# Kernel tuning notes

Measured on AMD Instinct MI355X. Metric: run time of the kernel, lower is better.

Reference implementation:

```python
import jax, jax.numpy as jnp
import numpy as np

N_POINTS = 8388608  # 8M points


def setup_inputs() -> dict:
    key = jax.random.key(0)
    k1, k2 = jax.random.split(key)
    pcloud = jax.random.normal(k1, (1, N_POINTS, 3), dtype=jnp.float32)
    P1 = jax.random.normal(k2, (3,), dtype=jnp.float32)
    return {"pcloud": pcloud, "P1": P1, "K": 64}


def reference(pcloud, P1, K):
    # pcloud: (1, N, 3) -> (N, 3); P1: (3,) -> (1, 3)
    pts = pcloud.reshape(-1, 3)
    diff = pts - P1.reshape(1, 3)
    dist = jnp.sqrt(jnp.sum(diff * diff, axis=1))  # L2 distance per point, (N,)
    # torch.topk(largest=False) == top_k on negated distances
    _, idx = jax.lax.top_k(-dist, K)  # (K,)
    return pts[idx], idx.reshape(1, -1)
```

## Files before the change

kernel.cpp:

```cpp
#include <hip/hip_runtime.h>
#include <stdint.h>

#define NBINS 4096
#define NB2   4096
#define NBLK  2048
#define SLOT  16
#define OVF_CAP 8192
#define LDS_CAND 8192
#define SAMP_PTS 131072
#define SBLK 128
#define CHUNK_PTS 256
#define CHUNK_F4  192

__device__ __forceinline__ uint32_t dist_key(float x, float y, float z,
                                             float px, float py, float pz) {
    float dx = __fsub_rn(x, px);
    float dy = __fsub_rn(y, py);
    float dz = __fsub_rn(z, pz);
    float s = __fadd_rn(__fadd_rn(__fmul_rn(dx, dx), __fmul_rn(dy, dy)),
                        __fmul_rn(dz, dz));
    float d = __fsqrt_rn(s);
    return __float_as_uint(d);
}

__global__ void __launch_bounds__(256) sample_scan_kernel(
        const float* __restrict__ pts, const float* __restrict__ P1,
        uint32_t* __restrict__ ghist, uint32_t* __restrict__ cutp,
        uint32_t* __restrict__ done_s, int nsamp, int K) {
    __shared__ uint32_t lh[NBINS];
    __shared__ uint32_t ssum[256];
    __shared__ int is_last;
    for (int i = threadIdx.x; i < NBINS; i += 256) lh[i] = 0;
    __syncthreads();
    float px = P1[0], py = P1[1], pz = P1[2];
    int gid = blockIdx.x * 256 + threadIdx.x;
    const float4* p4 = (const float4*)pts;
    if (gid * 4 < nsamp) {
        float4 A = p4[gid * 3 + 0];
        float4 Bv = p4[gid * 3 + 1];
        float4 Cv = p4[gid * 3 + 2];
        atomicAdd(&lh[dist_key(A.x, A.y, A.z, px, py, pz) >> 20], 1u);
        atomicAdd(&lh[dist_key(A.w, Bv.x, Bv.y, px, py, pz) >> 20], 1u);
        atomicAdd(&lh[dist_key(Bv.z, Bv.w, Cv.x, px, py, pz) >> 20], 1u);
        atomicAdd(&lh[dist_key(Cv.y, Cv.z, Cv.w, px, py, pz) >> 20], 1u);
    }
    __syncthreads();
    for (int i = threadIdx.x; i < NBINS; i += 256) {
        uint32_t v = lh[i];
        if (v) atomicAdd(&ghist[i], v);
    }
    __syncthreads();
    if (threadIdx.x == 0) {
        asm volatile("s_waitcnt vmcnt(0)" ::: "memory");
        uint32_t old = __hip_atomic_fetch_add(done_s, 1u, __ATOMIC_RELAXED,
                                              __HIP_MEMORY_SCOPE_AGENT);
        is_last = (old == (uint32_t)(gridDim.x - 1));
    }
    __syncthreads();
    if (!is_last) return;

    int t = threadIdx.x;
    uint32_t mine[16];
    uint32_t local = 0;
    for (int j = 0; j < 16; ++j) {
        mine[j] = __hip_atomic_load(&ghist[t * 16 + j], __ATOMIC_RELAXED,
                                    __HIP_MEMORY_SCOPE_AGENT);
        local += mine[j];
    }
    ssum[t] = local;
    __syncthreads();
    for (int off = 1; off < 256; off <<= 1) {
        uint32_t v = (t >= off) ? ssum[t - off] : 0;
        __syncthreads();
        ssum[t] += v;
        __syncthreads();
    }
    uint32_t incl = ssum[t];
    uint32_t excl = incl - local;
    if (excl < (uint32_t)K && incl >= (uint32_t)K) {
        uint32_t run = excl;
        for (int j = 0; j < 16; ++j) {
            run += mine[j];
            if (run >= (uint32_t)K) { *cutp = (uint32_t)(t * 16 + j); break; }
        }
    }
}

__global__ void __launch_bounds__(256) filter_kernel(
        const float* __restrict__ pts, const float* __restrict__ P1,
        const uint32_t* __restrict__ cutp,
        unsigned long long* __restrict__ gslots,
        uint32_t* __restrict__ gcount,
        uint32_t* __restrict__ ovf_cnt, unsigned long long* __restrict__ ovf,
        int nchunks, int N) {
    __shared__ float4 park[4][CHUNK_F4];
    __shared__ unsigned long long lhits[SLOT];
    __shared__ uint32_t lcnt;
    if (threadIdx.x == 0) lcnt = 0;
    __syncthreads();

    const float4* p4 = (const float4*)pts;
    float px = P1[0], py = P1[1], pz = P1[2];
    uint32_t cb = *cutp;
    int w = threadIdx.x >> 6;
    int lane = threadIdx.x & 63;
    int b = blockIdx.x;
    int cpb = (nchunks + NBLK - 1) / NBLK;
    int cbeg = b * cpb;
    int cend = cbeg + cpb; if (cend > nchunks) cend = nchunks;

    float4 a0, a1, a2, b0, b1, b2;
    int c = cbeg + w;
    bool hasA = (c < cend);
    if (hasA) {
        const float4* s = p4 + (size_t)c * CHUNK_F4;
        a0 = s[lane]; a1 = s[lane + 64]; a2 = s[lane + 128];
    }
    bool hasB = (c + 4 < cend);
    if (hasB) {
        const float4* s = p4 + (size_t)(c + 4) * CHUNK_F4;
        b0 = s[lane]; b1 = s[lane + 64]; b2 = s[lane + 128];
    }
    while (hasA) {
        park[w][lane] = a0; park[w][lane + 64] = a1; park[w][lane + 128] = a2;
        bool loadA = (c + 8 < cend);
        if (loadA) {
            const float4* s = p4 + (size_t)(c + 8) * CHUNK_F4;
            a0 = s[lane]; a1 = s[lane + 64]; a2 = s[lane + 128];
        }
        asm volatile("s_waitcnt lgkmcnt(0)" ::: "memory");
        {
            const float* fb = (const float*)&park[w][0] + lane * 12;
            float4 A  = *(const float4*)(fb);
            float4 Bv = *(const float4*)(fb + 4);
            float4 Cv = *(const float4*)(fb + 8);
            uint32_t kk[4];
            kk[0] = dist_key(A.x, A.y, A.z, px, py, pz);
            kk[1] = dist_key(A.w, Bv.x, Bv.y, px, py, pz);
            kk[2] = dist_key(Bv.z, Bv.w, Cv.x, px, py, pz);
            kk[3] = dist_key(Cv.y, Cv.z, Cv.w, px, py, pz);
            uint32_t pbase = (uint32_t)c * CHUNK_PTS + (uint32_t)lane * 4;
            #pragma unroll
            for (int j = 0; j < 4; ++j) {
                if ((kk[j] >> 20) <= cb) {
                    unsigned long long cv = ((unsigned long long)kk[j] << 32) |
                                            (unsigned long long)(pbase + j);
                    uint32_t pos = atomicAdd(&lcnt, 1u);
                    if (pos < SLOT) lhits[pos] = cv;
                    else {
                        uint32_t op = atomicAdd(ovf_cnt, 1u);
                        if (op < OVF_CAP) ovf[op] = cv;
                    }
                }
            }
        }
        bool loadB = false;
        if (hasB) {
            park[w][lane] = b0; park[w][lane + 64] = b1; park[w][lane + 128] = b2;
            loadB = (c + 12 < cend);
            if (loadB) {
                const float4* s = p4 + (size_t)(c + 12) * CHUNK_F4;
                b0 = s[lane]; b1 = s[lane + 64]; b2 = s[lane + 128];
            }
            asm volatile("s_waitcnt lgkmcnt(0)" ::: "memory");
            const float* fb = (const float*)&park[w][0] + lane * 12;
            float4 A  = *(const float4*)(fb);
            float4 Bv = *(const float4*)(fb + 4);
            float4 Cv = *(const float4*)(fb + 8);
            uint32_t kk[4];
            kk[0] = dist_key(A.x, A.y, A.z, px, py, pz);
            kk[1] = dist_key(A.w, Bv.x, Bv.y, px, py, pz);
            kk[2] = dist_key(Bv.z, Bv.w, Cv.x, px, py, pz);
            kk[3] = dist_key(Cv.y, Cv.z, Cv.w, px, py, pz);
            uint32_t pbase = (uint32_t)(c + 4) * CHUNK_PTS + (uint32_t)lane * 4;
            #pragma unroll
            for (int j = 0; j < 4; ++j) {
                if ((kk[j] >> 20) <= cb) {
                    unsigned long long cv = ((unsigned long long)kk[j] << 32) |
                                            (unsigned long long)(pbase + j);
                    uint32_t pos = atomicAdd(&lcnt, 1u);
                    if (pos < SLOT) lhits[pos] = cv;
                    else {
                        uint32_t op = atomicAdd(ovf_cnt, 1u);
                        if (op < OVF_CAP) ovf[op] = cv;
                    }
                }
            }
        }
        c += 8;
        hasA = (c < cend);
        hasB = loadB;
    }
    if (b == NBLK - 1 && threadIdx.x == 0) {
        for (int i = nchunks * CHUNK_PTS; i < N; ++i) {
            uint32_t kk = dist_key(pts[3 * i], pts[3 * i + 1], pts[3 * i + 2], px, py, pz);
            if ((kk >> 20) <= cb) {
                unsigned long long cv = ((unsigned long long)kk << 32) |
                                        (unsigned long long)(uint32_t)i;
                uint32_t pos = atomicAdd(&lcnt, 1u);
                if (pos < SLOT) lhits[pos] = cv;
                else {
                    uint32_t op = atomicAdd(ovf_cnt, 1u);
                    if (op < OVF_CAP) ovf[op] = cv;
                }
            }
        }
    }
    __syncthreads();
    uint32_t n = lcnt; if (n > SLOT) n = SLOT;
    if (threadIdx.x < n) gslots[(size_t)b * SLOT + threadIdx.x] = lhits[threadIdx.x];
    if (threadIdx.x == 0) gcount[b] = n;
}

__global__ void __launch_bounds__(1024) refine_select_kernel(
        const uint32_t* __restrict__ gcount,
        const unsigned long long* __restrict__ gslots,
        const uint32_t* __restrict__ ovf_cnt,
        const unsigned long long* __restrict__ ovf,
        const uint32_t* __restrict__ cutp,
        unsigned long long* __restrict__ cand2,
        const float* __restrict__ pts,
        float* __restrict__ out, int K) {
    __shared__ uint32_t hist2[NB2];
    __shared__ uint32_t ssum[1024];
    __shared__ unsigned long long lcand[LDS_CAND];
    __shared__ uint32_t cut2_s, m2_s;
    int t = threadIdx.x;
    uint32_t cb = *cutp;
    unsigned long long R = ((unsigned long long)(cb + 1)) << 20;
    uint32_t M32 = (uint32_t)((((unsigned long long)NB2) << 32) / R);
    uint32_t novf = *ovf_cnt; if (novf > OVF_CAP) novf = OVF_CAP;

    for (int i = t; i < NB2; i += 1024) hist2[i] = 0;
    if (t == 0) { m2_s = 0; cut2_s = NB2 - 1; }
    __syncthreads();
    for (int b = t; b < NBLK; b += 1024) {
        uint32_t n = gcount[b]; if (n > SLOT) n = SLOT;
        for (uint32_t j = 0; j < n; ++j) {
            uint32_t key = (uint32_t)(gslots[(size_t)b * SLOT + j] >> 32);
            atomicAdd(&hist2[(uint32_t)(((unsigned long long)key * M32) >> 32)], 1u);
        }
    }
    for (uint32_t i = t; i < novf; i += 1024) {
        uint32_t key = (uint32_t)(ovf[i] >> 32);
        atomicAdd(&hist2[(uint32_t)(((unsigned long long)key * M32) >> 32)], 1u);
    }
    __syncthreads();

    uint32_t mine[4];
    uint32_t local = 0;
    for (int j = 0; j < 4; ++j) { mine[j] = hist2[t * 4 + j]; local += mine[j]; }
    ssum[t] = local;
    __syncthreads();
    for (int off = 1; off < 1024; off <<= 1) {
        uint32_t v = (t >= off) ? ssum[t - off] : 0;
        __syncthreads();
        ssum[t] += v;
        __syncthreads();
    }
    uint32_t incl = ssum[t], excl = incl - local;
    if (excl < (uint32_t)K && incl >= (uint32_t)K) {
        uint32_t run = excl;
        for (int j = 0; j < 4; ++j) {
            run += mine[j];
            if (run >= (uint32_t)K) { cut2_s = (uint32_t)(t * 4 + j); break; }
        }
    }
    __syncthreads();
    uint32_t c2 = cut2_s;

    for (int b = t; b < NBLK; b += 1024) {
        uint32_t n = gcount[b]; if (n > SLOT) n = SLOT;
        for (uint32_t j = 0; j < n; ++j) {
            unsigned long long cv = gslots[(size_t)b * SLOT + j];
            uint32_t key = (uint32_t)(cv >> 32);
            if ((uint32_t)(((unsigned long long)key * M32) >> 32) <= c2) {
                uint32_t pos = atomicAdd(&m2_s, 1u);
                if (pos < LDS_CAND) lcand[pos] = cv;
                cand2[pos] = cv;
            }
        }
    }
    for (uint32_t i = t; i < novf; i += 1024) {
        unsigned long long cv = ovf[i];
        uint32_t key = (uint32_t)(cv >> 32);
        if ((uint32_t)(((unsigned long long)key * M32) >> 32) <= c2) {
            uint32_t pos = atomicAdd(&m2_s, 1u);
            if (pos < LDS_CAND) lcand[pos] = cv;
            cand2[pos] = cv;
        }
    }
    __syncthreads();
    uint32_t M2 = m2_s;

    if (M2 <= LDS_CAND) {
        for (uint32_t i = t; i < M2; i += 1024) {
            unsigned long long ci = lcand[i];
            uint32_t rank = 0;
            for (uint32_t j = 0; j < M2; ++j) rank += (lcand[j] < ci) ? 1u : 0u;
            if (rank < (uint32_t)K) {
                uint32_t idx = (uint32_t)(ci & 0xFFFFFFFFu);
                out[3 * rank + 0] = pts[3 * idx + 0];
                out[3 * rank + 1] = pts[3 * idx + 1];
                out[3 * rank + 2] = pts[3 * idx + 2];
                out[3 * K + rank] = (float)idx;
            }
        }
    } else {
        for (uint32_t i = t; i < M2; i += 1024) {
            unsigned long long ci = cand2[i];
            uint32_t rank = 0;
            for (uint32_t j = 0; j < M2; ++j) rank += (cand2[j] < ci) ? 1u : 0u;
            if (rank < (uint32_t)K) {
                uint32_t idx = (uint32_t)(ci & 0xFFFFFFFFu);
                out[3 * rank + 0] = pts[3 * idx + 0];
                out[3 * rank + 1] = pts[3 * idx + 1];
                out[3 * rank + 2] = pts[3 * idx + 2];
                out[3 * K + rank] = (float)idx;
            }
        }
    }
}

extern "C" void kernel_launch(void* const* d_in, const int* in_sizes, int n_in,
                              void* d_out, int out_size, void* d_ws, size_t ws_size,
                              hipStream_t stream) {
    const float* pts = (const float*)d_in[0];
    const float* P1  = (const float*)d_in[1];
    float* out = (float*)d_out;

    int N = in_sizes[0] / 3;
    int nchunks = N / CHUNK_PTS;
    int K = out_size / 4;
    int nsamp = (N < SAMP_PTS) ? (N / 4) * 4 : SAMP_PTS;

    uint32_t* w       = (uint32_t*)d_ws;
    uint32_t* ovf_cnt = w + 0;
    uint32_t* cutp    = w + 1;
    uint32_t* done_s  = w + 2;
    uint32_t* hist    = w + 4;
    uint32_t* gcount  = w + 4 + NBINS;
    unsigned long long* gslots = (unsigned long long*)(w + 4 + NBINS + NBLK);
    unsigned long long* ovf    = gslots + (size_t)NBLK * SLOT;
    unsigned long long* cand2  = ovf + OVF_CAP;

    hipMemsetAsync(w, 0, (size_t)(4 + NBINS) * sizeof(uint32_t), stream);
    sample_scan_kernel<<<SBLK, 256, 0, stream>>>(pts, P1, hist, cutp, done_s, nsamp, K);
    filter_kernel<<<NBLK, 256, 0, stream>>>(pts, P1, cutp, gslots, gcount,
                                            ovf_cnt, ovf, nchunks, N);
    refine_select_kernel<<<1, 1024, 0, stream>>>(gcount, gslots, ovf_cnt, ovf,
                                                 cutp, cand2, pts, out, K);
}
```

Baseline: 47.94 us.

## Stream filter chunks via direct global-to-LDS loads with triple-buffered ring

Replaces the register-staged double-buffered loads in the filter kernel with direct global-to-LDS loads into a per-wave three-slot ring, synchronised with vmcnt waits. This drops the register round trip and the explicit LDS stores, and keeps two chunks in flight while the current one is processed. It raises LDS use per block and relies on exact vmcnt accounting and on the wave-uniform LDS addressing semantics of the load-to-LDS instruction.

```diff
diff --git a/kernel.cpp b/kernel.cpp
--- a/kernel.cpp
+++ b/kernel.cpp
@@ -11,6 +11,9 @@
 #define SBLK 128
 #define CHUNK_PTS 256
 #define CHUNK_F4  192
+
+typedef const __attribute__((address_space(1))) void* gas_ptr;
+typedef __attribute__((address_space(3))) void* las_ptr;
 
 __device__ __forceinline__ uint32_t dist_key(float x, float y, float z,
                                              float px, float py, float pz) {
@@ -93,7 +96,7 @@
         uint32_t* __restrict__ gcount,
         uint32_t* __restrict__ ovf_cnt, unsigned long long* __restrict__ ovf,
         int nchunks, int N) {
-    __shared__ float4 park[4][CHUNK_F4];
+    __shared__ float4 ring[4][3][CHUNK_F4];
     __shared__ unsigned long long lhits[SLOT];
     __shared__ uint32_t lcnt;
     if (threadIdx.x == 0) lcnt = 0;
@@ -109,87 +112,50 @@
     int cbeg = b * cpb;
     int cend = cbeg + cpb; if (cend > nchunks) cend = nchunks;
 
-    float4 a0, a1, a2, b0, b1, b2;
-    int c = cbeg + w;
-    bool hasA = (c < cend);
-    if (hasA) {
-        const float4* s = p4 + (size_t)c * CHUNK_F4;
-        a0 = s[lane]; a1 = s[lane + 64]; a2 = s[lane + 128];
-    }
-    bool hasB = (c + 4 < cend);
-    if (hasB) {
-        const float4* s = p4 + (size_t)(c + 4) * CHUNK_F4;
-        b0 = s[lane]; b1 = s[lane + 64]; b2 = s[lane + 128];
-    }
-    while (hasA) {
-        park[w][lane] = a0; park[w][lane + 64] = a1; park[w][lane + 128] = a2;
-        bool loadA = (c + 8 < cend);
-        if (loadA) {
-            const float4* s = p4 + (size_t)(c + 8) * CHUNK_F4;
-            a0 = s[lane]; a1 = s[lane + 64]; a2 = s[lane + 128];
-        }
-        asm volatile("s_waitcnt lgkmcnt(0)" ::: "memory");
-        {
-            const float* fb = (const float*)&park[w][0] + lane * 12;
-            float4 A  = *(const float4*)(fb);
-            float4 Bv = *(const float4*)(fb + 4);
-            float4 Cv = *(const float4*)(fb + 8);
-            uint32_t kk[4];
-            kk[0] = dist_key(A.x, A.y, A.z, px, py, pz);
-            kk[1] = dist_key(A.w, Bv.x, Bv.y, px, py, pz);
-            kk[2] = dist_key(Bv.z, Bv.w, Cv.x, px, py, pz);
-            kk[3] = dist_key(Cv.y, Cv.z, Cv.w, px, py, pz);
-            uint32_t pbase = (uint32_t)c * CHUNK_PTS + (uint32_t)lane * 4;
-            #pragma unroll
-            for (int j = 0; j < 4; ++j) {
-                if ((kk[j] >> 20) <= cb) {
-                    unsigned long long cv = ((unsigned long long)kk[j] << 32) |
-                                            (unsigned long long)(pbase + j);
-                    uint32_t pos = atomicAdd(&lcnt, 1u);
-                    if (pos < SLOT) lhits[pos] = cv;
-                    else {
-                        uint32_t op = atomicAdd(ovf_cnt, 1u);
-                        if (op < OVF_CAP) ovf[op] = cv;
-                    }
+    int tiles = 0;
+    if (cend > cbeg + w) tiles = (cend - (cbeg + w) + 3) / 4;
+
+    auto stage = [&](int buf, int i) {
+        const float4* s = p4 + (size_t)(cbeg + w + 4 * i) * CHUNK_F4 + lane;
+        float4* d = &ring[w][buf][0];
+        __builtin_amdgcn_global_load_lds((gas_ptr)(s),       (las_ptr)(d),       16, 0, 0);
+        __builtin_amdgcn_global_load_lds((gas_ptr)(s + 64),  (las_ptr)(d + 64),  16, 0, 0);
+        __builtin_amdgcn_global_load_lds((gas_ptr)(s + 128), (las_ptr)(d + 128), 16, 0, 0);
+    };
+
+    if (tiles > 0) stage(0, 0);
+    if (tiles > 1) stage(1, 1);
+
+    for (int i = 0; i < tiles; ++i) {
+        if (i + 2 < tiles) stage((i + 2) % 3, i + 2);
+        if (i + 2 < tiles)      asm volatile("s_waitcnt vmcnt(6)" ::: "memory");
+        else if (i + 1 < tiles) asm volatile("s_waitcnt vmcnt(3)" ::: "memory");
+        else                    asm volatile("s_waitcnt vmcnt(0)" ::: "memory");
+        __builtin_amdgcn_sched_barrier(0);
+
+        const float* fb = (const float*)&ring[w][i % 3][0] + lane * 12;
+        float4 A  = *(const float4*)(fb);
+        float4 Bv = *(const float4*)(fb + 4);
+        float4 Cv = *(const float4*)(fb + 8);
+        uint32_t kk[4];
+        kk[0] = dist_key(A.x, A.y, A.z, px, py, pz);
+        kk[1] = dist_key(A.w, Bv.x, Bv.y, px, py, pz);
+        kk[2] = dist_key(Bv.z, Bv.w, Cv.x, px, py, pz);
+        kk[3] = dist_key(Cv.y, Cv.z, Cv.w, px, py, pz);
+        uint32_t pbase = (uint32_t)(cbeg + w + 4 * i) * CHUNK_PTS + (uint32_t)lane * 4;
+        #pragma unroll
+        for (int j = 0; j < 4; ++j) {
+            if ((kk[j] >> 20) <= cb) {
+                unsigned long long cv = ((unsigned long long)kk[j] << 32) |
+                                        (unsigned long long)(pbase + j);
+                uint32_t pos = atomicAdd(&lcnt, 1u);
+                if (pos < SLOT) lhits[pos] = cv;
+                else {
+                    uint32_t op = atomicAdd(ovf_cnt, 1u);
+                    if (op < OVF_CAP) ovf[op] = cv;
                 }
             }
         }
-        bool loadB = false;
-        if (hasB) {
-            park[w][lane] = b0; park[w][lane + 64] = b1; park[w][lane + 128] = b2;
-            loadB = (c + 12 < cend);
-            if (loadB) {
-                const float4* s = p4 + (size_t)(c + 12) * CHUNK_F4;
-                b0 = s[lane]; b1 = s[lane + 64]; b2 = s[lane + 128];
-            }
-            asm volatile("s_waitcnt lgkmcnt(0)" ::: "memory");
-            const float* fb = (const float*)&park[w][0] + lane * 12;
-            float4 A  = *(const float4*)(fb);
-            float4 Bv = *(const float4*)(fb + 4);
-            float4 Cv = *(const float4*)(fb + 8);
-            uint32_t kk[4];
-            kk[0] = dist_key(A.x, A.y, A.z, px, py, pz);
-            kk[1] = dist_key(A.w, Bv.x, Bv.y, px, py, pz);
-            kk[2] = dist_key(Bv.z, Bv.w, Cv.x, px, py, pz);
-            kk[3] = dist_key(Cv.y, Cv.z, Cv.w, px, py, pz);
-            uint32_t pbase = (uint32_t)(c + 4) * CHUNK_PTS + (uint32_t)lane * 4;
-            #pragma unroll
-            for (int j = 0; j < 4; ++j) {
-                if ((kk[j] >> 20) <= cb) {
-                    unsigned long long cv = ((unsigned long long)kk[j] << 32) |
-                                            (unsigned long long)(pbase + j);
-                    uint32_t pos = atomicAdd(&lcnt, 1u);
-                    if (pos < SLOT) lhits[pos] = cv;
-                    else {
-                        uint32_t op = atomicAdd(ovf_cnt, 1u);
-                        if (op < OVF_CAP) ovf[op] = cv;
-                    }
-                }
-            }
-        }
-        c += 8;
-        hasA = (c < cend);
-        hasB = loadB;
     }
     if (b == NBLK - 1 && threadIdx.x == 0) {
         for (int i = nchunks * CHUNK_PTS; i < N; ++i) {
```

After: 47.19 us. Within noise of the previous version (-1.6%).
